# Optimization experiments

Hardware: AMD Instinct MI355X
Metric: run time of the kernel (lower is better)

Reference implementation:

```python
import jax, jax.numpy as jnp
import numpy as np

B, S, H, D = 4, 1024, 20, 64
DM = H * D          # 1280 model dim
DF = 4 * DM         # 5120 ffn dim
EPS = 1e-5          # haiku LayerNorm default


def setup_inputs() -> dict:
    key = jax.random.key(0)
    ks = jax.random.split(key, 12)
    sc = 1.0 / np.sqrt(DM)
    return {
        "x": jax.random.normal(ks[0], (B, S, DM), jnp.float32),
        "ln1_scale": jnp.ones((DM,), jnp.float32),
        "ln1_offset": jnp.zeros((DM,), jnp.float32),
        "wq": jax.random.normal(ks[1], (DM, DM), jnp.float32) * sc,
        "bq": jnp.zeros((DM,), jnp.float32),
        "wk": jax.random.normal(ks[2], (DM, DM), jnp.float32) * sc,
        "bk": jnp.zeros((DM,), jnp.float32),
        "wv": jax.random.normal(ks[3], (DM, DM), jnp.float32) * sc,
        "bv": jnp.zeros((DM,), jnp.float32),
        "wo": jax.random.normal(ks[4], (DM, DM), jnp.float32) * sc,
        "bo": jnp.zeros((DM,), jnp.float32),
        "ln2_scale": jnp.ones((DM,), jnp.float32),
        "ln2_offset": jnp.zeros((DM,), jnp.float32),
        "fc1_w": jax.random.normal(ks[5], (DM, DF), jnp.float32) * sc,
        "fc1_b": jnp.zeros((DF,), jnp.float32),
        "fc2_w": jax.random.normal(ks[6], (DF, DM), jnp.float32) * (1.0 / np.sqrt(DF)),
        "fc2_b": jnp.zeros((DM,), jnp.float32),
    }


def _layer_norm(x, scale, offset):
    m = jnp.mean(x, axis=-1, keepdims=True)
    v = jnp.mean(jnp.square(x - m), axis=-1, keepdims=True)
    return (x - m) * jax.lax.rsqrt(v + EPS) * scale + offset


def reference(x, ln1_scale, ln1_offset, wq, bq, wk, bk, wv, bv, wo, bo,
              ln2_scale, ln2_offset, fc1_w, fc1_b, fc2_w, fc2_b):
    b, s, dm = x.shape
    # --- self-attention sub-block ---
    res = x
    h = _layer_norm(x, ln1_scale, ln1_offset)
    q = (h @ wq + bq).reshape(b, s, H, D)
    k = (h @ wk + bk).reshape(b, s, H, D)
    v = (h @ wv + bv).reshape(b, s, H, D)
    logits = jnp.einsum('bthd,bThd->bhtT', q, k) / jnp.sqrt(jnp.asarray(D, x.dtype))
    weights = jax.nn.softmax(logits, axis=-1)
    attn = jnp.einsum('bhtT,bThd->bthd', weights, v).reshape(b, s, dm)
    x = res + (attn @ wo + bo)
    # --- MLP sub-block ---
    res = x
    h = _layer_norm(x, ln2_scale, ln2_offset)
    h = jax.nn.gelu(h @ fc1_w + fc1_b, approximate=False)
    x = res + (h @ fc2_w + fc2_b)
    return x
```

## Files before the change

kernel.cpp:

```cpp
#include <hip/hip_runtime.h>
#include <hip/hip_bf16.h>

typedef __hip_bfloat16 bf16;
typedef __attribute__((ext_vector_type(8))) short short8;
typedef __attribute__((ext_vector_type(4))) float f32x4;

#define DMODEL 1280
#define DFFN   5120
#define BATCH  4
#define SEQ    1024
#define NHEAD  20
#define HDIM   64
#define NROWS  (BATCH * SEQ)

#define GLDS(g, l) __builtin_amdgcn_global_load_lds(                            \
    (const __attribute__((address_space(1))) void*)(g),                         \
    (__attribute__((address_space(3))) void*)(l), 16, 0, 0)

__global__ __launch_bounds__(256) void transpose_cvt(
    const float* __restrict__ in, bf16* __restrict__ out, int K, int N)
{
    __shared__ float tile[32][33];
    const int n0 = blockIdx.x * 32;
    const int k0 = blockIdx.y * 32;
    const int tx = threadIdx.x;
    const int ty = threadIdx.y;
    for (int i = 0; i < 32; i += 8)
        tile[ty + i][tx] = in[(size_t)(k0 + ty + i) * N + (n0 + tx)];
    __syncthreads();
    for (int i = 0; i < 32; i += 8)
        out[(size_t)(n0 + ty + i) * K + (k0 + tx)] = __float2bfloat16(tile[tx][ty + i]);
}

__global__ __launch_bounds__(256) void transpose_cvt4(
    const float* __restrict__ s0, const float* __restrict__ s1,
    const float* __restrict__ s2, const float* __restrict__ s3,
    bf16* __restrict__ d0, bf16* __restrict__ d1,
    bf16* __restrict__ d2, bf16* __restrict__ d3)
{
    __shared__ float tile[32][33];
    const float* in;
    bf16* out;
    switch (blockIdx.z) {
        case 0: in = s0; out = d0; break;
        case 1: in = s1; out = d1; break;
        case 2: in = s2; out = d2; break;
        default: in = s3; out = d3; break;
    }
    const int n0 = blockIdx.x * 32;
    const int k0 = blockIdx.y * 32;
    const int tx = threadIdx.x;
    const int ty = threadIdx.y;
    for (int i = 0; i < 32; i += 8)
        tile[ty + i][tx] = in[(size_t)(k0 + ty + i) * DMODEL + (n0 + tx)];
    __syncthreads();
    for (int i = 0; i < 32; i += 8)
        out[(size_t)(n0 + ty + i) * DMODEL + (k0 + tx)] = __float2bfloat16(tile[tx][ty + i]);
}

__global__ __launch_bounds__(256) void pack_bias3(
    const float* __restrict__ a, const float* __restrict__ b,
    const float* __restrict__ c, float* __restrict__ o)
{
    const int i = blockIdx.x * 256 + threadIdx.x;
    if (i < DMODEL) {
        o[i] = a[i];
        o[DMODEL + i] = b[i];
        o[2 * DMODEL + i] = c[i];
    }
}

__global__ __launch_bounds__(256) void ln_bf16(
    const float* __restrict__ x, const float* __restrict__ sc,
    const float* __restrict__ of, bf16* __restrict__ out)
{
    const int row = blockIdx.x;
    const float* xr = x + (size_t)row * DMODEL;
    float v[5];
    float s = 0.f, s2 = 0.f;
    for (int i = 0; i < 5; ++i) {
        v[i] = xr[threadIdx.x + i * 256];
        s += v[i];
        s2 += v[i] * v[i];
    }
    for (int off = 1; off < 64; off <<= 1) {
        s  += __shfl_xor(s, off);
        s2 += __shfl_xor(s2, off);
    }
    __shared__ float red[2][4];
    const int wid = threadIdx.x >> 6;
    if ((threadIdx.x & 63) == 0) { red[0][wid] = s; red[1][wid] = s2; }
    __syncthreads();
    s  = red[0][0] + red[0][1] + red[0][2] + red[0][3];
    s2 = red[1][0] + red[1][1] + red[1][2] + red[1][3];
    const float mean = s * (1.0f / DMODEL);
    const float var  = s2 * (1.0f / DMODEL) - mean * mean;
    const float rstd = rsqrtf(var + 1e-5f);
    for (int i = 0; i < 5; ++i) {
        const int c = threadIdx.x + i * 256;
        const float y = (v[i] - mean) * rstd * sc[c] + of[c];
        out[(size_t)row * DMODEL + c] = __float2bfloat16(y);
    }
}

__global__ __launch_bounds__(256) void reduce2_ln(
    const float* __restrict__ P, const float* __restrict__ bias,
    const float* __restrict__ res, float* __restrict__ x1,
    const float* __restrict__ sc, const float* __restrict__ of,
    bf16* __restrict__ h2)
{
    const int row = blockIdx.x;
    const size_t base = (size_t)row * DMODEL;
    const int MN = NROWS * DMODEL;
    float v[5];
    float s = 0.f, s2 = 0.f;
    for (int i = 0; i < 5; ++i) {
        const int c = threadIdx.x + i * 256;
        const float val = P[base + c] + P[MN + base + c] + bias[c] + res[base + c];
        v[i] = val;
        x1[base + c] = val;
        s += val;
        s2 += val * val;
    }
    for (int off = 1; off < 64; off <<= 1) {
        s  += __shfl_xor(s, off);
        s2 += __shfl_xor(s2, off);
    }
    __shared__ float red[2][4];
    const int wid = threadIdx.x >> 6;
    if ((threadIdx.x & 63) == 0) { red[0][wid] = s; red[1][wid] = s2; }
    __syncthreads();
    s  = red[0][0] + red[0][1] + red[0][2] + red[0][3];
    s2 = red[1][0] + red[1][1] + red[1][2] + red[1][3];
    const float mean = s * (1.0f / DMODEL);
    const float var  = s2 * (1.0f / DMODEL) - mean * mean;
    const float rstd = rsqrtf(var + 1e-5f);
    for (int i = 0; i < 5; ++i) {
        const int c = threadIdx.x + i * 256;
        const float y = (v[i] - mean) * rstd * sc[c] + of[c];
        h2[base + c] = __float2bfloat16(y);
    }
}

template <int EPI>
__global__ __launch_bounds__(256) void gemm_bf16(
    const bf16* __restrict__ A, const bf16* __restrict__ Bt,
    const float* __restrict__ bias,
    bf16* __restrict__ Cb, float* __restrict__ Cf,
    int M, int N, int K, int klen)
{
    __shared__ bf16 As[2][128][64];
    __shared__ bf16 Bs[2][128][64];
    const int m0 = blockIdx.x * 128;
    const int n0 = blockIdx.y * 128;
    const int z  = blockIdx.z;
    const int kbeg = z * klen;

    const int tid  = threadIdx.x;
    const int lane = tid & 63;
    const int wid  = tid >> 6;
    const int wm   = (wid >> 1) * 64;
    const int wn   = (wid & 1) * 64;
    const int l15  = lane & 15;
    const int lq   = lane >> 4;
    const int l7   = l15 & 7;

    f32x4 acc[4][4];
    for (int i = 0; i < 4; ++i)
        for (int j = 0; j < 4; ++j)
            acc[i][j] = (f32x4){0.f, 0.f, 0.f, 0.f};

    const int srow = lane >> 3;
    const int cgl  = ((lane & 7) ^ srow) * 8;
    const int lrow = wid * 8 + srow;
    const int lcol = (lane & 7) * 8;

    const bf16* aT = A  + (size_t)(m0 + lrow) * K + kbeg + cgl;
    const bf16* bT = Bt + (size_t)(n0 + lrow) * K + kbeg + cgl;
    const size_t rstep = (size_t)32 * K;

    for (int i = 0; i < 4; ++i) GLDS(aT + i * rstep, &As[0][lrow + i * 32][lcol]);
    for (int i = 0; i < 4; ++i) GLDS(bT + i * rstep, &Bs[0][lrow + i * 32][lcol]);

    const int nIter = klen / 64;
    for (int it = 0; it < nIter; ++it) {
        const int buf = it & 1;
        __syncthreads();
        if (it + 1 < nIter) {
            const int k1 = (it + 1) * 64;
            for (int i = 0; i < 4; ++i)
                GLDS(aT + k1 + i * rstep, &As[buf ^ 1][lrow + i * 32][lcol]);
            for (int i = 0; i < 4; ++i)
                GLDS(bT + k1 + i * rstep, &Bs[buf ^ 1][lrow + i * 32][lcol]);
        }
        for (int ko = 0; ko < 2; ++ko) {
            const int ca = ((ko * 4 + lq) ^ l7) * 8;
            short8 af[4], bfr[4];
            for (int mt = 0; mt < 4; ++mt)
                af[mt] = *(const short8*)(&As[buf][wm + mt * 16 + l15][ca]);
            for (int nt = 0; nt < 4; ++nt)
                bfr[nt] = *(const short8*)(&Bs[buf][wn + nt * 16 + l15][ca]);
            for (int mt = 0; mt < 4; ++mt)
                for (int nt = 0; nt < 4; ++nt)
                    acc[mt][nt] = __builtin_amdgcn_mfma_f32_16x16x32_bf16(
                        af[mt], bfr[nt], acc[mt][nt], 0, 0, 0);
        }
    }

    float* Pf = Cf + (size_t)z * M * N;
    for (int mt = 0; mt < 4; ++mt)
        for (int nt = 0; nt < 4; ++nt)
            for (int r = 0; r < 4; ++r) {
                const int row = m0 + wm + mt * 16 + lq * 4 + r;
                const int col = n0 + wn + nt * 16 + l15;
                if (EPI == 0) {
                    const float v = acc[mt][nt][r] + bias[col];
                    Cb[(size_t)row * N + col] = __float2bfloat16(v);
                } else if (EPI == 2) {
                    const float v = acc[mt][nt][r] + bias[col];
                    const float g = 0.5f * v * (1.0f + erff(v * 0.70710678118654752f));
                    Cb[(size_t)row * N + col] = __float2bfloat16(g);
                } else {
                    Pf[(size_t)row * N + col] = acc[mt][nt][r];
                }
            }
}

__global__ __launch_bounds__(256) void reduce2(
    const float* __restrict__ P, const float* __restrict__ bias,
    const float* __restrict__ res, float* __restrict__ out, int MN, int N)
{
    const int i = (blockIdx.x * 256 + threadIdx.x) * 4;
    if (i >= MN) return;
    const float4 p0 = *(const float4*)(P + i);
    const float4 p1 = *(const float4*)(P + MN + i);
    const float4 r  = *(const float4*)(res + i);
    const float4 b  = *(const float4*)(bias + (i % N));
    float4 o;
    o.x = p0.x + p1.x + r.x + b.x;
    o.y = p0.y + p1.y + r.y + b.y;
    o.z = p0.z + p1.z + r.z + b.z;
    o.w = p0.w + p1.w + r.w + b.w;
    *(float4*)(out + i) = o;
}

__global__ __launch_bounds__(256) void flash_attn(
    const bf16* __restrict__ qb, const bf16* __restrict__ kb,
    const bf16* __restrict__ vb, bf16* __restrict__ ob, int ldq)
{
    __shared__ bf16 Ks[64][72];
    __shared__ bf16 Vt[64][72];
    __shared__ bf16 Ps[4][16][72];

    const int bh = blockIdx.y;
    const int b  = bh / NHEAD;
    const int hh = bh % NHEAD;
    const int q0 = blockIdx.x * 64;
    const int tid  = threadIdx.x;
    const int lane = tid & 63;
    const int wid  = tid >> 6;
    const int l15  = lane & 15;
    const int lq   = lane >> 4;

    short8 qf[2];
    {
        const bf16* qp = qb + ((size_t)(b * SEQ + q0 + wid * 16 + l15) * ldq)
                         + hh * HDIM + lq * 8;
        for (int kk = 0; kk < 2; ++kk) {
            union { short8 v; bf16 h[8]; } u;
            u.v = *(const short8*)(qp + kk * 32);
            for (int j = 0; j < 8; ++j)
                u.h[j] = __float2bfloat16(__bfloat162float(u.h[j]) * 0.125f);
            qf[kk] = u.v;
        }
    }

    float m_r[4] = {-INFINITY, -INFINITY, -INFINITY, -INFINITY};
    float l_r[4] = {0.f, 0.f, 0.f, 0.f};
    f32x4 o[4];
    for (int nt = 0; nt < 4; ++nt) o[nt] = (f32x4){0.f, 0.f, 0.f, 0.f};

    const int srow = tid >> 2;
    const int scol = (tid & 3) * 16;

    for (int j0 = 0; j0 < SEQ; j0 += 64) {
        const size_t gbase = (size_t)(b * SEQ + j0 + srow) * ldq + hh * HDIM + scol;
        uint4 kv0 = *(const uint4*)(kb + gbase);
        uint4 kv1 = *(const uint4*)(kb + gbase + 8);
        uint4 vv0 = *(const uint4*)(vb + gbase);
        uint4 vv1 = *(const uint4*)(vb + gbase + 8);
        __syncthreads();
        *(uint4*)(&Ks[srow][scol])     = kv0;
        *(uint4*)(&Ks[srow][scol + 8]) = kv1;
        {
            union { uint4 u[2]; bf16 h[16]; } tv;
            tv.u[0] = vv0; tv.u[1] = vv1;
            for (int i = 0; i < 16; ++i) Vt[scol + i][srow] = tv.h[i];
        }
        __syncthreads();

        f32x4 s[4];
        for (int nt = 0; nt < 4; ++nt) {
            f32x4 a = (f32x4){0.f, 0.f, 0.f, 0.f};
            for (int kk = 0; kk < 2; ++kk) {
                short8 kf = *(const short8*)(&Ks[nt * 16 + l15][lq * 8 + kk * 32]);
                a = __builtin_amdgcn_mfma_f32_16x16x32_bf16(qf[kk], kf, a, 0, 0, 0);
            }
            s[nt] = a;
        }

        for (int r = 0; r < 4; ++r) {
            float mx = fmaxf(fmaxf(s[0][r], s[1][r]), fmaxf(s[2][r], s[3][r]));
            for (int off = 1; off < 16; off <<= 1) mx = fmaxf(mx, __shfl_xor(mx, off));
            const float mnew  = fmaxf(m_r[r], mx);
            const float alpha = __expf(m_r[r] - mnew);
            float rs = 0.f;
            for (int nt = 0; nt < 4; ++nt) {
                const float p = __expf(s[nt][r] - mnew);
                s[nt][r] = p;
                rs += p;
            }
            for (int off = 1; off < 16; off <<= 1) rs += __shfl_xor(rs, off);
            l_r[r] = l_r[r] * alpha + rs;
            m_r[r] = mnew;
            for (int nt = 0; nt < 4; ++nt) o[nt][r] *= alpha;
        }

        for (int nt = 0; nt < 4; ++nt)
            for (int r = 0; r < 4; ++r)
                Ps[wid][lq * 4 + r][l15 + nt * 16] = __float2bfloat16(s[nt][r]);
        __syncthreads();

        for (int kk = 0; kk < 2; ++kk) {
            const short8 pf = *(const short8*)(&Ps[wid][l15][lq * 8 + kk * 32]);
            for (int nt = 0; nt < 4; ++nt) {
                const short8 vf = *(const short8*)(&Vt[l15 + nt * 16][lq * 8 + kk * 32]);
                o[nt] = __builtin_amdgcn_mfma_f32_16x16x32_bf16(pf, vf, o[nt], 0, 0, 0);
            }
        }
    }

    for (int r = 0; r < 4; ++r) {
        const float inv_l = 1.0f / l_r[r];
        const int row = q0 + wid * 16 + lq * 4 + r;
        for (int nt = 0; nt < 4; ++nt) {
            const int col = hh * HDIM + l15 + nt * 16;
            ob[(size_t)(b * SEQ + row) * DMODEL + col] =
                __float2bfloat16(o[nt][r] * inv_l);
        }
    }
}

extern "C" void kernel_launch(void* const* d_in, const int* in_sizes, int n_in,
                              void* d_out, int out_size, void* d_ws, size_t ws_size,
                              hipStream_t stream)
{
    (void)in_sizes; (void)n_in; (void)out_size; (void)ws_size;
    const float* x    = (const float*)d_in[0];
    const float* ln1s = (const float*)d_in[1];
    const float* ln1o = (const float*)d_in[2];
    const float* wq   = (const float*)d_in[3];
    const float* bq   = (const float*)d_in[4];
    const float* wk   = (const float*)d_in[5];
    const float* bk   = (const float*)d_in[6];
    const float* wv   = (const float*)d_in[7];
    const float* bv   = (const float*)d_in[8];
    const float* wo   = (const float*)d_in[9];
    const float* bo   = (const float*)d_in[10];
    const float* ln2s = (const float*)d_in[11];
    const float* ln2o = (const float*)d_in[12];
    const float* fc1w = (const float*)d_in[13];
    const float* fc1b = (const float*)d_in[14];
    const float* fc2w = (const float*)d_in[15];
    const float* fc2b = (const float*)d_in[16];
    float* out = (float*)d_out;

    char* wp = (char*)d_ws;
    auto alloc = [&](size_t n) { char* p = wp; wp += (n + 255) & ~(size_t)255; return p; };
    bf16*  wqkvt = (bf16*)alloc((size_t)3 * DMODEL * DMODEL * 2);
    bf16*  wot   = (bf16*)alloc((size_t)DMODEL * DMODEL * 2);
    bf16*  fc1t  = (bf16*)alloc((size_t)DFFN * DMODEL * 2);
    bf16*  fc2t  = (bf16*)alloc((size_t)DMODEL * DFFN * 2);
    float* bqkv  = (float*)alloc((size_t)3 * DMODEL * 4);
    char*  regA  = alloc((size_t)NROWS * DMODEL * 2
                       + (size_t)NROWS * 3 * DMODEL * 2
                       + (size_t)NROWS * DMODEL * 2);
    bf16*  h     = (bf16*)regA;
    bf16*  qkv   = (bf16*)(regA + (size_t)NROWS * DMODEL * 2);
    bf16*  attn  = (bf16*)(regA + (size_t)NROWS * 4 * DMODEL * 2);
    float* part  = (float*)regA;
    bf16*  h2    = (bf16*)alloc((size_t)NROWS * DMODEL * 2);
    bf16*  g     = (bf16*)alloc((size_t)NROWS * DFFN * 2);
    float* x1    = out;

    const dim3 tb(32, 8);
    transpose_cvt4<<<dim3(DMODEL / 32, DMODEL / 32, 4), tb, 0, stream>>>(
        wq, wk, wv, wo,
        wqkvt, wqkvt + (size_t)DMODEL * DMODEL, wqkvt + (size_t)2 * DMODEL * DMODEL, wot);
    transpose_cvt<<<dim3(DFFN / 32, DMODEL / 32), tb, 0, stream>>>(fc1w, fc1t, DMODEL, DFFN);
    transpose_cvt<<<dim3(DMODEL / 32, DFFN / 32), tb, 0, stream>>>(fc2w, fc2t, DFFN, DMODEL);
    pack_bias3<<<(DMODEL + 255) / 256, 256, 0, stream>>>(bq, bk, bv, bqkv);

    ln_bf16<<<NROWS, 256, 0, stream>>>(x, ln1s, ln1o, h);

    gemm_bf16<0><<<dim3(NROWS / 128, 3 * DMODEL / 128, 1), 256, 0, stream>>>(
        h, wqkvt, bqkv, qkv, nullptr, NROWS, 3 * DMODEL, DMODEL, DMODEL);

    flash_attn<<<dim3(SEQ / 64, BATCH * NHEAD), 256, 0, stream>>>(
        qkv, qkv + DMODEL, qkv + 2 * DMODEL, attn, 3 * DMODEL);

    gemm_bf16<3><<<dim3(NROWS / 128, DMODEL / 128, 2), 256, 0, stream>>>(
        attn, wot, nullptr, nullptr, part, NROWS, DMODEL, DMODEL, DMODEL / 2);
    reduce2_ln<<<NROWS, 256, 0, stream>>>(part, bo, x, x1, ln2s, ln2o, h2);

    gemm_bf16<2><<<dim3(NROWS / 128, DFFN / 128, 1), 256, 0, stream>>>(
        h2, fc1t, fc1b, g, nullptr, NROWS, DFFN, DMODEL, DMODEL);

    gemm_bf16<3><<<dim3(NROWS / 128, DMODEL / 128, 2), 256, 0, stream>>>(
        g, fc2t, nullptr, nullptr, part, NROWS, DMODEL, DFFN, DFFN / 2);
    reduce2<<<(NROWS * DMODEL / 4 + 255) / 256, 256, 0, stream>>>(
        part, fc2b, x1, out, NROWS * DMODEL, DMODEL);
}
```

Before: 536.5 us.

## Halve GEMM K-tile for occupancy and restructure flash attention with prefetch

The GEMM now uses a 32-wide K tile with a 4-way XOR swizzle and launch_bounds(256,4), cutting LDS per block so more blocks fit on a CU, at the cost of twice as many barriers per K. Flash attention now processes 128 query rows per block (two 16-row tiles per wave), so each K/V tile loaded is reused across more queries. It also double-buffers K via async global-to-LDS loads, prefetches V into registers for the next tile, and swizzles the Ks, Vt and Ps layouts instead of padding them. Together these aim to reduce global traffic and LDS bank conflicts in attention and improve GEMM latency hiding, but they raise register pressure and halve the attention grid.

```diff
diff --git a/kernel.cpp b/kernel.cpp
--- a/kernel.cpp
+++ b/kernel.cpp
@@ -4,6 +4,7 @@
 typedef __hip_bfloat16 bf16;
 typedef __attribute__((ext_vector_type(8))) short short8;
 typedef __attribute__((ext_vector_type(4))) float f32x4;
+typedef __attribute__((ext_vector_type(4))) unsigned short u16x4;
 
 #define DMODEL 1280
 #define DFFN   5120
@@ -143,14 +144,14 @@
 }
 
 template <int EPI>
-__global__ __launch_bounds__(256) void gemm_bf16(
+__global__ __launch_bounds__(256, 4) void gemm_bf16(
     const bf16* __restrict__ A, const bf16* __restrict__ Bt,
     const float* __restrict__ bias,
     bf16* __restrict__ Cb, float* __restrict__ Cf,
     int M, int N, int K, int klen)
 {
-    __shared__ bf16 As[2][128][64];
-    __shared__ bf16 Bs[2][128][64];
+    __shared__ bf16 As[2][128][32];
+    __shared__ bf16 Bs[2][128][32];
     const int m0 = blockIdx.x * 128;
     const int n0 = blockIdx.y * 128;
     const int z  = blockIdx.z;
@@ -163,48 +164,48 @@
     const int wn   = (wid & 1) * 64;
     const int l15  = lane & 15;
     const int lq   = lane >> 4;
-    const int l7   = l15 & 7;
 
     f32x4 acc[4][4];
     for (int i = 0; i < 4; ++i)
         for (int j = 0; j < 4; ++j)
             acc[i][j] = (f32x4){0.f, 0.f, 0.f, 0.f};
 
-    const int srow = lane >> 3;
-    const int cgl  = ((lane & 7) ^ srow) * 8;
-    const int lrow = wid * 8 + srow;
-    const int lcol = (lane & 7) * 8;
-
-    const bf16* aT = A  + (size_t)(m0 + lrow) * K + kbeg + cgl;
-    const bf16* bT = Bt + (size_t)(n0 + lrow) * K + kbeg + cgl;
-    const size_t rstep = (size_t)32 * K;
-
-    for (int i = 0; i < 4; ++i) GLDS(aT + i * rstep, &As[0][lrow + i * 32][lcol]);
-    for (int i = 0; i < 4; ++i) GLDS(bT + i * rstep, &Bs[0][lrow + i * 32][lcol]);
-
-    const int nIter = klen / 64;
+    const int srow = lane >> 2;
+    const int cph  = lane & 3;
+    const int cgl8 = (cph ^ (srow & 3)) * 8;
+    const int lrow = wid * 16 + srow;
+    const int lcol = cph * 8;
+
+    const bf16* aT = A  + (size_t)(m0 + lrow) * K + kbeg + cgl8;
+    const bf16* bT = Bt + (size_t)(n0 + lrow) * K + kbeg + cgl8;
+    const size_t rstep = (size_t)64 * K;
+
+    GLDS(aT,         &As[0][lrow][lcol]);
+    GLDS(aT + rstep, &As[0][lrow + 64][lcol]);
+    GLDS(bT,         &Bs[0][lrow][lcol]);
+    GLDS(bT + rstep, &Bs[0][lrow + 64][lcol]);
+
+    const int ca = (lq ^ (l15 & 3)) * 8;
+    const int nIter = klen / 32;
     for (int it = 0; it < nIter; ++it) {
         const int buf = it & 1;
         __syncthreads();
         if (it + 1 < nIter) {
-            const int k1 = (it + 1) * 64;
-            for (int i = 0; i < 4; ++i)
-                GLDS(aT + k1 + i * rstep, &As[buf ^ 1][lrow + i * 32][lcol]);
-            for (int i = 0; i < 4; ++i)
-                GLDS(bT + k1 + i * rstep, &Bs[buf ^ 1][lrow + i * 32][lcol]);
-        }
-        for (int ko = 0; ko < 2; ++ko) {
-            const int ca = ((ko * 4 + lq) ^ l7) * 8;
-            short8 af[4], bfr[4];
-            for (int mt = 0; mt < 4; ++mt)
-                af[mt] = *(const short8*)(&As[buf][wm + mt * 16 + l15][ca]);
+            const int k1 = (it + 1) * 32;
+            GLDS(aT + k1,         &As[buf ^ 1][lrow][lcol]);
+            GLDS(aT + k1 + rstep, &As[buf ^ 1][lrow + 64][lcol]);
+            GLDS(bT + k1,         &Bs[buf ^ 1][lrow][lcol]);
+            GLDS(bT + k1 + rstep, &Bs[buf ^ 1][lrow + 64][lcol]);
+        }
+        short8 af[4], bfr[4];
+        for (int mt = 0; mt < 4; ++mt)
+            af[mt] = *(const short8*)(&As[buf][wm + mt * 16 + l15][ca]);
+        for (int nt = 0; nt < 4; ++nt)
+            bfr[nt] = *(const short8*)(&Bs[buf][wn + nt * 16 + l15][ca]);
+        for (int mt = 0; mt < 4; ++mt)
             for (int nt = 0; nt < 4; ++nt)
-                bfr[nt] = *(const short8*)(&Bs[buf][wn + nt * 16 + l15][ca]);
-            for (int mt = 0; mt < 4; ++mt)
-                for (int nt = 0; nt < 4; ++nt)
-                    acc[mt][nt] = __builtin_amdgcn_mfma_f32_16x16x32_bf16(
-                        af[mt], bfr[nt], acc[mt][nt], 0, 0, 0);
-        }
+                acc[mt][nt] = __builtin_amdgcn_mfma_f32_16x16x32_bf16(
+                    af[mt], bfr[nt], acc[mt][nt], 0, 0, 0);
     }
 
     float* Pf = Cf + (size_t)z * M * N;
@@ -248,107 +249,145 @@
     const bf16* __restrict__ qb, const bf16* __restrict__ kb,
     const bf16* __restrict__ vb, bf16* __restrict__ ob, int ldq)
 {
-    __shared__ bf16 Ks[64][72];
-    __shared__ bf16 Vt[64][72];
-    __shared__ bf16 Ps[4][16][72];
+    __shared__ bf16 Ks[2][64][64];
+    __shared__ bf16 Vt[64][64];
+    __shared__ bf16 Ps[4][32][64];
 
     const int bh = blockIdx.y;
     const int b  = bh / NHEAD;
     const int hh = bh % NHEAD;
-    const int q0 = blockIdx.x * 64;
+    const int q0 = blockIdx.x * 128;
     const int tid  = threadIdx.x;
     const int lane = tid & 63;
     const int wid  = tid >> 6;
     const int l15  = lane & 15;
     const int lq   = lane >> 4;
-
-    short8 qf[2];
-    {
-        const bf16* qp = qb + ((size_t)(b * SEQ + q0 + wid * 16 + l15) * ldq)
+    const int key  = l15 & 7;
+
+    short8 qf[2][2];
+    for (int mt = 0; mt < 2; ++mt) {
+        const bf16* qp = qb + (size_t)(b * SEQ + q0 + wid * 32 + mt * 16 + l15) * ldq
                          + hh * HDIM + lq * 8;
         for (int kk = 0; kk < 2; ++kk) {
             union { short8 v; bf16 h[8]; } u;
             u.v = *(const short8*)(qp + kk * 32);
             for (int j = 0; j < 8; ++j)
                 u.h[j] = __float2bfloat16(__bfloat162float(u.h[j]) * 0.125f);
-            qf[kk] = u.v;
-        }
-    }
-
-    float m_r[4] = {-INFINITY, -INFINITY, -INFINITY, -INFINITY};
-    float l_r[4] = {0.f, 0.f, 0.f, 0.f};
-    f32x4 o[4];
-    for (int nt = 0; nt < 4; ++nt) o[nt] = (f32x4){0.f, 0.f, 0.f, 0.f};
-
-    const int srow = tid >> 2;
-    const int scol = (tid & 3) * 16;
-
-    for (int j0 = 0; j0 < SEQ; j0 += 64) {
-        const size_t gbase = (size_t)(b * SEQ + j0 + srow) * ldq + hh * HDIM + scol;
-        uint4 kv0 = *(const uint4*)(kb + gbase);
-        uint4 kv1 = *(const uint4*)(kb + gbase + 8);
-        uint4 vv0 = *(const uint4*)(vb + gbase);
-        uint4 vv1 = *(const uint4*)(vb + gbase + 8);
+            qf[mt][kk] = u.v;
+        }
+    }
+
+    float m_r[2][4], l_r[2][4];
+    f32x4 o[2][4];
+    for (int mt = 0; mt < 2; ++mt)
+        for (int i = 0; i < 4; ++i) {
+            m_r[mt][i] = -INFINITY;
+            l_r[mt][i] = 0.f;
+            o[mt][i] = (f32x4){0.f, 0.f, 0.f, 0.f};
+        }
+
+    const int krow  = wid * 8 + (lane >> 3);
+    const int kcgl8 = ((lane & 7) ^ (krow & 7)) * 8;
+    const int kcph8 = (lane & 7) * 8;
+    const int vd0  = (tid & 15) * 4;
+    const int vkv0 = (tid >> 4) * 4;
+
+    const bf16* kBase = kb + (size_t)(b * SEQ + krow) * ldq + hh * HDIM + kcgl8;
+    const bf16* vBase = vb + (size_t)(b * SEQ + vkv0) * ldq + hh * HDIM + vd0;
+
+    GLDS(kBase,                        &Ks[0][krow][kcph8]);
+    GLDS(kBase + (size_t)32 * ldq,     &Ks[0][krow + 32][kcph8]);
+    u16x4 vr[4];
+    for (int j = 0; j < 4; ++j)
+        vr[j] = *(const u16x4*)(vBase + (size_t)j * ldq);
+
+    const int nIter = SEQ / 64;
+    for (int it = 0; it < nIter; ++it) {
+        const int buf = it & 1;
         __syncthreads();
-        *(uint4*)(&Ks[srow][scol])     = kv0;
-        *(uint4*)(&Ks[srow][scol + 8]) = kv1;
-        {
-            union { uint4 u[2]; bf16 h[16]; } tv;
-            tv.u[0] = vv0; tv.u[1] = vv1;
-            for (int i = 0; i < 16; ++i) Vt[scol + i][srow] = tv.h[i];
+        for (int i = 0; i < 4; ++i) {
+            u16x4 w = { vr[0][i], vr[1][i], vr[2][i], vr[3][i] };
+            const int p = ((vkv0 >> 3) ^ ((vd0 + i) & 7)) * 8 + (vkv0 & 7);
+            *(u16x4*)(&Vt[vd0 + i][p]) = w;
         }
         __syncthreads();
 
-        f32x4 s[4];
+        if (it + 1 < nIter) {
+            const size_t koff = (size_t)(it + 1) * 64 * ldq;
+            GLDS(kBase + koff,                    &Ks[buf ^ 1][krow][kcph8]);
+            GLDS(kBase + koff + (size_t)32 * ldq, &Ks[buf ^ 1][krow + 32][kcph8]);
+            const size_t voff = (size_t)(it + 1) * 64 * ldq;
+            for (int j = 0; j < 4; ++j)
+                vr[j] = *(const u16x4*)(vBase + voff + (size_t)j * ldq);
+        }
+
+        f32x4 s[2][4];
         for (int nt = 0; nt < 4; ++nt) {
-            f32x4 a = (f32x4){0.f, 0.f, 0.f, 0.f};
-            for (int kk = 0; kk < 2; ++kk) {
-                short8 kf = *(const short8*)(&Ks[nt * 16 + l15][lq * 8 + kk * 32]);
-                a = __builtin_amdgcn_mfma_f32_16x16x32_bf16(qf[kk], kf, a, 0, 0, 0);
+            const bf16* krow_p = &Ks[buf][nt * 16 + l15][0];
+            const short8 kf0 = *(const short8*)(krow_p + ((lq + 0) ^ key) * 8);
+            const short8 kf1 = *(const short8*)(krow_p + ((lq + 4) ^ key) * 8);
+            for (int mt = 0; mt < 2; ++mt) {
+                f32x4 a = (f32x4){0.f, 0.f, 0.f, 0.f};
+                a = __builtin_amdgcn_mfma_f32_16x16x32_bf16(qf[mt][0], kf0, a, 0, 0, 0);
+                a = __builtin_amdgcn_mfma_f32_16x16x32_bf16(qf[mt][1], kf1, a, 0, 0, 0);
+                s[mt][nt] = a;
             }
-            s[nt] = a;
-        }
-
+        }
+
+        for (int mt = 0; mt < 2; ++mt)
+            for (int r = 0; r < 4; ++r) {
+                float mx = fmaxf(fmaxf(s[mt][0][r], s[mt][1][r]),
+                                 fmaxf(s[mt][2][r], s[mt][3][r]));
+                for (int off = 1; off < 16; off <<= 1)
+                    mx = fmaxf(mx, __shfl_xor(mx, off));
+                const float mnew  = fmaxf(m_r[mt][r], mx);
+                const float alpha = __expf(m_r[mt][r] - mnew);
+                float rs = 0.f;
+                for (int nt = 0; nt < 4; ++nt) {
+                    const float p = __expf(s[mt][nt][r] - mnew);
+                    s[mt][nt][r] = p;
+                    rs += p;
+                }
+                for (int off = 1; off < 16; off <<= 1)
+                    rs += __shfl_xor(rs, off);
+                l_r[mt][r] = l_r[mt][r] * alpha + rs;
+                m_r[mt][r] = mnew;
+                for (int nt = 0; nt < 4; ++nt) o[mt][nt][r] *= alpha;
+            }
+
+        for (int mt = 0; mt < 2; ++mt)
+            for (int nt = 0; nt < 4; ++nt)
+                for (int r = 0; r < 4; ++r) {
+                    const int prow = mt * 16 + lq * 4 + r;
+                    const int pc = (((l15 >> 3) + nt * 2) ^ (prow & 7)) * 8 + (l15 & 7);
+                    Ps[wid][prow][pc] = __float2bfloat16(s[mt][nt][r]);
+                }
+
+        for (int kk = 0; kk < 2; ++kk) {
+            short8 pf[2];
+            for (int mt = 0; mt < 2; ++mt)
+                pf[mt] = *(const short8*)(
+                    &Ps[wid][mt * 16 + l15][((lq + 4 * kk) ^ key) * 8]);
+            for (int nt = 0; nt < 4; ++nt) {
+                const short8 vf = *(const short8*)(
+                    &Vt[nt * 16 + l15][((lq + 4 * kk) ^ key) * 8]);
+                for (int mt = 0; mt < 2; ++mt)
+                    o[mt][nt] = __builtin_amdgcn_mfma_f32_16x16x32_bf16(
+                        pf[mt], vf, o[mt][nt], 0, 0, 0);
+            }
+        }
+    }
+
+    for (int mt = 0; mt < 2; ++mt)
         for (int r = 0; r < 4; ++r) {
-            float mx = fmaxf(fmaxf(s[0][r], s[1][r]), fmaxf(s[2][r], s[3][r]));
-            for (int off = 1; off < 16; off <<= 1) mx = fmaxf(mx, __shfl_xor(mx, off));
-            const float mnew  = fmaxf(m_r[r], mx);
-            const float alpha = __expf(m_r[r] - mnew);
-            float rs = 0.f;
+            const float inv_l = 1.0f / l_r[mt][r];
+            const int row = q0 + wid * 32 + mt * 16 + lq * 4 + r;
             for (int nt = 0; nt < 4; ++nt) {
-                const float p = __expf(s[nt][r] - mnew);
-                s[nt][r] = p;
-                rs += p;
+                const int col = hh * HDIM + l15 + nt * 16;
+                ob[(size_t)(b * SEQ + row) * DMODEL + col] =
+                    __float2bfloat16(o[mt][nt][r] * inv_l);
             }
-            for (int off = 1; off < 16; off <<= 1) rs += __shfl_xor(rs, off);
-            l_r[r] = l_r[r] * alpha + rs;
-            m_r[r] = mnew;
-            for (int nt = 0; nt < 4; ++nt) o[nt][r] *= alpha;
-        }
-
-        for (int nt = 0; nt < 4; ++nt)
-            for (int r = 0; r < 4; ++r)
-                Ps[wid][lq * 4 + r][l15 + nt * 16] = __float2bfloat16(s[nt][r]);
-        __syncthreads();
-
-        for (int kk = 0; kk < 2; ++kk) {
-            const short8 pf = *(const short8*)(&Ps[wid][l15][lq * 8 + kk * 32]);
-            for (int nt = 0; nt < 4; ++nt) {
-                const short8 vf = *(const short8*)(&Vt[l15 + nt * 16][lq * 8 + kk * 32]);
-                o[nt] = __builtin_amdgcn_mfma_f32_16x16x32_bf16(pf, vf, o[nt], 0, 0, 0);
-            }
-        }
-    }
-
-    for (int r = 0; r < 4; ++r) {
-        const float inv_l = 1.0f / l_r[r];
-        const int row = q0 + wid * 16 + lq * 4 + r;
-        for (int nt = 0; nt < 4; ++nt) {
-            const int col = hh * HDIM + l15 + nt * 16;
-            ob[(size_t)(b * SEQ + row) * DMODEL + col] =
-                __float2bfloat16(o[nt][r] * inv_l);
-        }
-    }
+        }
 }
 
 extern "C" void kernel_launch(void* const* d_in, const int* in_sizes, int n_in,
@@ -406,7 +445,7 @@
     gemm_bf16<0><<<dim3(NROWS / 128, 3 * DMODEL / 128, 1), 256, 0, stream>>>(
         h, wqkvt, bqkv, qkv, nullptr, NROWS, 3 * DMODEL, DMODEL, DMODEL);
 
-    flash_attn<<<dim3(SEQ / 64, BATCH * NHEAD), 256, 0, stream>>>(
+    flash_attn<<<dim3(SEQ / 128, BATCH * NHEAD), 256, 0, stream>>>(
         qkv, qkv + DMODEL, qkv + 2 * DMODEL, attn, 3 * DMODEL);
 
     gemm_bf16<3><<<dim3(NROWS / 128, DMODEL / 128, 2), 256, 0, stream>>>(
```

Measured after the change: 526.8 us. Within noise of the previous version (-1.8%).
